# Kernel optimization log

Measured on AMD Instinct MI355X. Metric: run time of the kernel, lower is better.

Reference implementation:

```python
import jax, jax.numpy as jnp
import numpy as np

N_QUBITS = 12
RANK = 1024
K = 4            # outcomes per qubit
D = 2 ** N_QUBITS
N_IDX = 1_000_000


def setup_inputs() -> dict:
    key = jax.random.key(0)
    k1, k2, k3, k4 = jax.random.split(key, 4)
    params = jax.random.normal(k1, (2, D, RANK), dtype=jnp.float32)
    M_real = jax.random.normal(k2, (K, 2, 2), dtype=jnp.float32)
    M_imag = jax.random.normal(k3, (K, 2, 2), dtype=jnp.float32)
    P_idxs = jax.random.randint(k4, (N_IDX,), 0, K ** N_QUBITS, dtype=jnp.int64)
    return {"params": params, "M_real": M_real, "M_imag": M_imag, "P_idxs": P_idxs}


def _qmt(rho, M, n_qubits):
    """Born rule: P[s1..sN] = Tr[(M_{s1} x ... x M_{sN}) rho].
    Sequential per-qubit contraction; T has shape [K^n, 2^(N-n), 2^(N-n)]."""
    T = rho[None, :, :]  # axes: (done outcomes, row legs j, col legs i)
    for _ in range(n_qubits):
        k, r, c = T.shape[0], T.shape[1] // 2, T.shape[2] // 2
        Tt = T.reshape(k, 2, r, 2, c)  # (k, j_n, j_rest, i_n, i_rest)
        # Tr contribution: sum_{i,j} M[s,i,j] * rho[j,i]
        T = jnp.einsum('sij,kjait->ksat', M, Tt).reshape(k * M.shape[0], r, c)
    return T.reshape(-1)  # [K^N] complex


def reference(params, M_real, M_imag, P_idxs):
    # rho = U U^H / Tr(U U^H)
    U = jax.lax.complex(params[0], params[1])            # [D, RANK] complex64
    rho = U @ U.conj().T                                  # [D, D]
    rho = rho / jnp.trace(rho)
    M = jax.lax.complex(M_real, M_imag)                   # [K, 2, 2] complex64
    P_all = _qmt(rho, M, N_QUBITS).real                   # [K^N] float32
    return P_all[P_idxs]
```

## Files before the change

### kernel.cpp

```cpp
#include <hip/hip_runtime.h>

#define D 4096
#define RANK 1024
#define UELEMS 4194304ULL
#define NTOT 16777216ULL
#define QSCALE 16000.0f

typedef __attribute__((ext_vector_type(4))) int i32x4;

__device__ float g_inv_tr[1];
__device__ float g_scale[D];
__device__ float g_mdre[16];
__device__ float g_mdim[16];

static __device__ __forceinline__ void load_lds16(const void* g, void* l) {
    __builtin_amdgcn_global_load_lds(
        (const __attribute__((address_space(1))) unsigned int*)g,
        (__attribute__((address_space(3))) unsigned int*)l, 16, 0, 0);
}

#define MFMA_I8 __builtin_amdgcn_mfma_i32_16x16x64_i8

__global__ __launch_bounds__(256) void convert_w_i8(const float* __restrict__ P,
                                                    const float* __restrict__ Mre,
                                                    const float* __restrict__ Mim,
                                                    char* __restrict__ Wh,
                                                    char* __restrict__ Wl,
                                                    char* __restrict__ W2)
{
    if (blockIdx.x == 0 && threadIdx.x < 16) {
        const int s = threadIdx.x >> 2, i = (threadIdx.x >> 1) & 1, j = threadIdx.x & 1;
        g_mdre[threadIdx.x] =  Mre[s * 4 + j * 2 + i];
        g_mdim[threadIdx.x] = -Mim[s * 4 + j * 2 + i];
    }

    const int w = threadIdx.x >> 6, lane = threadIdx.x & 63;
    const int row = blockIdx.x * 4 + w;

    float ur[16], ui[16];
    const float* pr = P + (size_t)row * RANK + lane * 16;
    const float* pi = P + UELEMS + (size_t)row * RANK + lane * 16;
    #pragma unroll
    for (int q = 0; q < 4; ++q) {
        const float4 a = ((const float4*)pr)[q];
        const float4 b = ((const float4*)pi)[q];
        ur[q * 4 + 0] = a.x; ur[q * 4 + 1] = a.y; ur[q * 4 + 2] = a.z; ur[q * 4 + 3] = a.w;
        ui[q * 4 + 0] = b.x; ui[q * 4 + 1] = b.y; ui[q * 4 + 2] = b.z; ui[q * 4 + 3] = b.w;
    }
    float mx = 0.f;
    #pragma unroll
    for (int e = 0; e < 16; ++e)
        mx = fmaxf(mx, fmaxf(fabsf(ur[e]), fabsf(ui[e])));
    #pragma unroll
    for (int off = 1; off < 64; off <<= 1)
        mx = fmaxf(mx, __shfl_xor(mx, off));
    const float inv = mx > 0.f ? QSCALE / mx : 0.f;
    if (lane == 0) g_scale[row] = mx / QSCALE;

    int hr[16], lr[16], hi[16], li[16];
    #pragma unroll
    for (int e = 0; e < 16; ++e) {
        float q = ur[e] * inv;
        float hf = rintf(q * 0.0078125f);
        hr[e] = (int)hf; lr[e] = (int)rintf(q - 128.f * hf);
        q = ui[e] * inv;
        hf = rintf(q * 0.0078125f);
        hi[e] = (int)hf; li[e] = (int)rintf(q - 128.f * hf);
    }
    uint4 phr, plr, phi, pli;
    unsigned* dst[4] = {(unsigned*)&phr, (unsigned*)&plr, (unsigned*)&phi, (unsigned*)&pli};
    #pragma unroll
    for (int q = 0; q < 4; ++q) {
        unsigned a = 0, b = 0, c = 0, d = 0;
        #pragma unroll
        for (int k = 0; k < 4; ++k) {
            const int sh = k * 8;
            a |= (unsigned)(hr[q * 4 + k] & 255) << sh;
            b |= (unsigned)(lr[q * 4 + k] & 255) << sh;
            c |= (unsigned)(hi[q * 4 + k] & 255) << sh;
            d |= (unsigned)(li[q * 4 + k] & 255) << sh;
        }
        dst[0][q] = a; dst[1][q] = b; dst[2][q] = c; dst[3][q] = d;
    }
    const size_t b1 = (size_t)row * 2048 + lane * 16;
    *(uint4*)&Wh[b1] = phr;          *(uint4*)&Wl[b1] = plr;
    *(uint4*)&Wh[b1 + 1024] = phi;   *(uint4*)&Wl[b1 + 1024] = pli;

    const size_t b2 = ((size_t)lane * 4096 + row) * 16;
    *(uint4*)&W2[b2]                = phr;
    *(uint4*)&W2[b2 + 4194304]      = plr;
    *(uint4*)&W2[b2 + 8388608]      = phi;
    *(uint4*)&W2[b2 + 12582912]     = pli;
}

__global__ __launch_bounds__(256, 2) void gemm_rho_i8(const char* __restrict__ Wh,
                                                      const char* __restrict__ Wl,
                                                      const char* __restrict__ W2,
                                                      float2* __restrict__ rho)
{
    __shared__ __align__(16) char sA[2][4][64 * 64];

    const int g0 = blockIdx.x;
    const int g = (g0 & 7) * 260 + (g0 >> 3);

    int bi = (int)((sqrtf(8.f * (float)g + 1.f) - 1.f) * 0.5f);
    while (bi * (bi + 1) / 2 > g) --bi;
    while ((bi + 1) * (bi + 2) / 2 <= g) ++bi;
    const int bj = g - bi * (bi + 1) / 2;
    const int row0 = bi << 6, col0 = bj << 6;

    const int t = threadIdx.x;
    const int lane = t & 63, w = t >> 6;
    const int wr = w >> 1, wc = w & 1;

    const int ra = t >> 2;
    const int kca = (t & 3) ^ ((ra >> 1) & 3);
    const size_t aoff = (size_t)(row0 + ra) * 2048 + kca * 16;
    const int ldso = t * 16;

    const int m = lane & 15, gq = lane >> 4;
    const int fko = (gq ^ ((m >> 1) & 3)) * 16;

    const size_t bcol = ((size_t)gq * 4096 + col0 + wc * 32 + m) * 16;

    i32x4 rehh[2][2], remx[2][2], iphh[2][2], ipmx[2][2], iqhh[2][2], iqmx[2][2];
    #pragma unroll
    for (int i = 0; i < 2; ++i)
        #pragma unroll
        for (int j = 0; j < 2; ++j) {
            rehh[i][j] = (i32x4){0, 0, 0, 0}; remx[i][j] = (i32x4){0, 0, 0, 0};
            iphh[i][j] = (i32x4){0, 0, 0, 0}; ipmx[i][j] = (i32x4){0, 0, 0, 0};
            iqhh[i][j] = (i32x4){0, 0, 0, 0}; iqmx[i][j] = (i32x4){0, 0, 0, 0};
        }

    char* const sA0 = &sA[0][0][0];

#define STAGE_A(bn, kt)                                                       \
    {                                                                         \
        const size_t ko_ = (size_t)(kt) * 64;                                 \
        char* dA_ = sA0 + (bn) * 16384;                                       \
        load_lds16(Wh + aoff + ko_,        dA_ + ldso);                       \
        load_lds16(Wl + aoff + ko_,        dA_ + 4096  + ldso);               \
        load_lds16(Wh + aoff + ko_ + 1024, dA_ + 8192  + ldso);               \
        load_lds16(Wl + aoff + ko_ + 1024, dA_ + 12288 + ldso);               \
    }

    STAGE_A(0, 0)
    __syncthreads();

    #pragma unroll 2
    for (int kt = 0; kt < 16; ++kt) {
        const int cur = kt & 1;
        const char* sAc = sA0 + cur * 16384;

        i32x4 b1h[2], b1l[2], b2h[2], b2l[2];
        {
            const char* pB = W2 + bcol + (size_t)kt * 262144;
            #pragma unroll
            for (int j = 0; j < 2; ++j) {
                b1h[j] = *(const i32x4*)(pB + j * 256);
                b1l[j] = *(const i32x4*)(pB + 4194304  + j * 256);
                b2h[j] = *(const i32x4*)(pB + 8388608  + j * 256);
                b2l[j] = *(const i32x4*)(pB + 12582912 + j * 256);
            }
        }

        if (kt < 15) STAGE_A(cur ^ 1, kt + 1)

        i32x4 fa1h[2], fa1l[2], fa2h[2], fa2l[2];
        #pragma unroll
        for (int i = 0; i < 2; ++i) {
            const int off = (wr * 32 + i * 16 + m) * 64 + fko;
            fa1h[i] = *(const i32x4*)(sAc + off);
            fa1l[i] = *(const i32x4*)(sAc + 4096  + off);
            fa2h[i] = *(const i32x4*)(sAc + 8192  + off);
            fa2l[i] = *(const i32x4*)(sAc + 12288 + off);
        }

        __builtin_amdgcn_s_setprio(1);
        #pragma unroll
        for (int j = 0; j < 2; ++j)
            #pragma unroll
            for (int i = 0; i < 2; ++i) {
                i32x4 r;
                r = rehh[i][j];
                r = MFMA_I8(fa1h[i], b1h[j], r, 0, 0, 0);
                r = MFMA_I8(fa2h[i], b2h[j], r, 0, 0, 0);
                rehh[i][j] = r;
                r = remx[i][j];
                r = MFMA_I8(fa1h[i], b1l[j], r, 0, 0, 0);
                r = MFMA_I8(fa1l[i], b1h[j], r, 0, 0, 0);
                r = MFMA_I8(fa2h[i], b2l[j], r, 0, 0, 0);
                r = MFMA_I8(fa2l[i], b2h[j], r, 0, 0, 0);
                remx[i][j] = r;
                r = MFMA_I8(fa2h[i], b1h[j], iphh[i][j], 0, 0, 0);
                iphh[i][j] = r;
                r = ipmx[i][j];
                r = MFMA_I8(fa2h[i], b1l[j], r, 0, 0, 0);
                r = MFMA_I8(fa2l[i], b1h[j], r, 0, 0, 0);
                ipmx[i][j] = r;
                r = MFMA_I8(fa1h[i], b2h[j], iqhh[i][j], 0, 0, 0);
                iqhh[i][j] = r;
                r = iqmx[i][j];
                r = MFMA_I8(fa1h[i], b2l[j], r, 0, 0, 0);
                r = MFMA_I8(fa1l[i], b2h[j], r, 0, 0, 0);
                iqmx[i][j] = r;
            }
        __builtin_amdgcn_s_setprio(0);

        __syncthreads();
    }
#undef STAGE_A

    #pragma unroll
    for (int j = 0; j < 2; ++j) {
        const int col = col0 + wc * 32 + j * 16 + m;
        const float sc = g_scale[col];
        const int c64 = col >> 6;
        #pragma unroll
        for (int i = 0; i < 2; ++i) {
            #pragma unroll
            for (int r = 0; r < 4; ++r) {
                const int row = row0 + wr * 32 + i * 16 + gq * 4 + r;
                const float s2 = g_scale[row] * sc;
                const float re = s2 * (16384.f * (float)rehh[i][j][r] + 128.f * (float)remx[i][j][r]);
                const float im = s2 * (16384.f * (float)(iphh[i][j][r] - iqhh[i][j][r])
                                      + 128.f * (float)(ipmx[i][j][r] - iqmx[i][j][r]));
                const int r64 = row >> 6;
                if (r64 > c64 || row >= col) rho[(size_t)row * D + col] = make_float2(re, im);
                if (r64 == c64 && row > col) rho[(size_t)col * D + row] = make_float2(re, -im);
            }
        }
    }
}

__global__ void trace_inv(const float2* __restrict__ rho)
{
    __shared__ float red[256];
    float s = 0.f;
    for (int d = threadIdx.x; d < D; d += 256)
        s += rho[(size_t)d * (D + 1)].x;
    red[threadIdx.x] = s;
    __syncthreads();
    for (int off = 128; off > 0; off >>= 1) {
        if (threadIdx.x < off) red[threadIdx.x] += red[threadIdx.x + off];
        __syncthreads();
    }
    if (threadIdx.x == 0) g_inv_tr[0] = 1.0f / red[0];
}

static __device__ __forceinline__ void qmt2(float2* x,
                                            const float* __restrict__ Mre,
                                            const float* __restrict__ Mim)
{
    float2 y[16];
    #pragma unroll
    for (int sb = 0; sb < 4; ++sb)
        #pragma unroll
        for (int ja = 0; ja < 2; ++ja)
            #pragma unroll
            for (int ia = 0; ia < 2; ++ia) {
                float2 acc = make_float2(0.f, 0.f);
                #pragma unroll
                for (int ib = 0; ib < 2; ++ib)
                    #pragma unroll
                    for (int jb = 0; jb < 2; ++jb) {
                        const float mr = Mre[sb * 4 + ib * 2 + jb];
                        const float mi = Mim[sb * 4 + ib * 2 + jb];
                        const float2 v = x[(ja * 2 + jb) * 4 + ia * 2 + ib];
                        acc.x += mr * v.x - mi * v.y;
                        acc.y += mr * v.y + mi * v.x;
                    }
                y[sb * 4 + ja * 2 + ia] = acc;
            }
    #pragma unroll
    for (int sa = 0; sa < 4; ++sa)
        #pragma unroll
        for (int sb = 0; sb < 4; ++sb) {
            float2 acc = make_float2(0.f, 0.f);
            #pragma unroll
            for (int ia = 0; ia < 2; ++ia)
                #pragma unroll
                for (int ja = 0; ja < 2; ++ja) {
                    const float mr = Mre[sa * 4 + ia * 2 + ja];
                    const float mi = Mim[sa * 4 + ia * 2 + ja];
                    const float2 v = y[sb * 4 + ja * 2 + ia];
                    acc.x += mr * v.x - mi * v.y;
                    acc.y += mr * v.y + mi * v.x;
                }
            x[sa * 4 + sb] = acc;
        }
}

static __device__ __forceinline__ void pA_pipeline(float2* x, float2* X, const int t,
                                                   const float* __restrict__ mre,
                                                   const float* __restrict__ mim)
{
    qmt2(x, mre, mim);
    #pragma unroll
    for (int d = 0; d < 16; ++d) X[t * 17 + d] = x[d];
    __syncthreads();
    const int a2 = t >> 6, t2 = (t >> 4) & 3, d1 = t & 15;
    #pragma unroll
    for (int j2 = 0; j2 < 4; ++j2)
        #pragma unroll
        for (int i2 = 0; i2 < 4; ++i2)
            x[j2 * 4 + i2] = X[((a2 * 4 + j2) * 16 + t2 * 4 + i2) * 17 + d1];
    __syncthreads();
    qmt2(x, mre, mim);
    #pragma unroll
    for (int d = 0; d < 16; ++d) X[(a2 * 4 + t2) * 257 + d * 16 + d1] = x[d];
    __syncthreads();
    const int e2 = t >> 4, e1 = t & 15;
    #pragma unroll
    for (int j2 = 0; j2 < 4; ++j2)
        #pragma unroll
        for (int i2 = 0; i2 < 4; ++i2)
            x[j2 * 4 + i2] = X[(j2 * 4 + i2) * 257 + e2 * 16 + e1];
    qmt2(x, mre, mim);
}

__global__ __launch_bounds__(256) void qmt_pAh(const float2* __restrict__ in,
                                               float2* __restrict__ out,
                                               const float* __restrict__ Mre,
                                               const float* __restrict__ Mim)
{
    __shared__ __align__(16) float2 X[256 * 17];
    const int t = threadIdx.x;
    const int g = blockIdx.x;
    int rr = (int)((sqrtf(8.f * (float)g + 1.f) - 1.f) * 0.5f);
    while (rr * (rr + 1) / 2 > g) --rr;
    while ((rr + 1) * (rr + 2) / 2 <= g) ++rr;
    const int cc = g - rr * (rr + 1) / 2;

    const int a4 = t >> 4, t4 = t & 15;
    float2 x0[16], x[16];
    #pragma unroll
    for (int j2 = 0; j2 < 4; ++j2) {
        const float2* p = in + ((size_t)(rr * 64 + a4 * 4 + j2)) * 4096 + cc * 64 + t4 * 4;
        const float4 v0 = ((const float4*)p)[0];
        const float4 v1 = ((const float4*)p)[1];
        x0[j2 * 4 + 0] = make_float2(v0.x, v0.y);
        x0[j2 * 4 + 1] = make_float2(v0.z, v0.w);
        x0[j2 * 4 + 2] = make_float2(v1.x, v1.y);
        x0[j2 * 4 + 3] = make_float2(v1.z, v1.w);
    }

    #pragma unroll
    for (int q = 0; q < 16; ++q) x[q] = x0[q];
    pA_pipeline(x, X, t, Mre, Mim);
    const int e2 = t >> 4, e1 = t & 15;
    const size_t ob0 = (size_t)(rr * 64 + cc) * 4096 + e2 * 16 + e1;
    #pragma unroll
    for (int d = 0; d < 16; ++d) out[ob0 + (size_t)d * 256] = x[d];

    if (rr != cc) {
        __syncthreads();
        #pragma unroll
        for (int q = 0; q < 16; ++q) x[q] = x0[q];
        pA_pipeline(x, X, t, g_mdre, g_mdim);
        const size_t ob1 = (size_t)(cc * 64 + rr) * 4096 + e2 * 16 + e1;
        #pragma unroll
        for (int d = 0; d < 16; ++d)
            out[ob1 + (size_t)d * 256] = make_float2(x[d].x, -x[d].y);
    }
}

static __device__ __forceinline__ void qmt_stage_cb_half(float2* x,
                                                         const float* __restrict__ Mre,
                                                         const float* __restrict__ Mim)
{
    #pragma unroll
    for (int jb = 0; jb < 2; ++jb) {
        float2 y[16];
        #pragma unroll
        for (int sc = 0; sc < 4; ++sc)
            #pragma unroll
            for (int ii = 0; ii < 4; ++ii) {
                float2 acc = make_float2(0.f, 0.f);
                #pragma unroll
                for (int ic = 0; ic < 2; ++ic)
                    #pragma unroll
                    for (int jc = 0; jc < 2; ++jc) {
                        const float mr = Mre[sc * 4 + ic * 2 + jc];
                        const float mi = Mim[sc * 4 + ic * 2 + jc];
                        const float2 v = x[jb * 16 + jc * 8 + ii * 2 + ic];
                        acc.x += mr * v.x - mi * v.y;
                        acc.y += mr * v.y + mi * v.x;
                    }
                y[sc * 4 + ii] = acc;
            }
        #pragma unroll
        for (int q = 0; q < 16; ++q) x[jb * 16 + q] = y[q];
    }
    #pragma unroll
    for (int sc = 0; sc < 4; ++sc) {
        float2 z[8];
        #pragma unroll
        for (int sb = 0; sb < 4; ++sb)
            #pragma unroll
            for (int ia = 0; ia < 2; ++ia) {
                float2 acc = make_float2(0.f, 0.f);
                #pragma unroll
                for (int ib = 0; ib < 2; ++ib)
                    #pragma unroll
                    for (int jb = 0; jb < 2; ++jb) {
                        const float mr = Mre[sb * 4 + ib * 2 + jb];
                        const float mi = Mim[sb * 4 + ib * 2 + jb];
                        const float2 v = x[jb * 16 + sc * 4 + ia * 2 + ib];
                        acc.x += mr * v.x - mi * v.y;
                        acc.y += mr * v.y + mi * v.x;
                    }
                z[sb * 2 + ia] = acc;
            }
        #pragma unroll
        for (int sb = 0; sb < 4; ++sb)
            #pragma unroll
            for (int ia = 0; ia < 2; ++ia)
                x[(sb >> 1) * 16 + sc * 4 + ia * 2 + (sb & 1)] = z[sb * 2 + ia];
    }
}

#define STAGE_A_COEFFS                                                        \
    float Are[2][2], Aim[2][2], Bre[2][2], Bim[2][2];                         \
    _Pragma("unroll")                                                         \
    for (int sal = 0; sal < 2; ++sal)                                         \
        _Pragma("unroll")                                                     \
        for (int ia = 0; ia < 2; ++ia) {                                      \
            const int sa = 2 * h + sal;                                       \
            Are[sal][ia] = Mre[sa * 4 + ia * 2 + h];                          \
            Aim[sal][ia] = Mim[sa * 4 + ia * 2 + h];                          \
            Bre[sal][ia] = Mre[sa * 4 + ia * 2 + (1 - h)];                    \
            Bim[sal][ia] = Mim[sa * 4 + ia * 2 + (1 - h)];                    \
        }

__global__ __launch_bounds__(256) void qmt_p3(const float2* __restrict__ in,
                                              float2* __restrict__ out,
                                              const float* __restrict__ Mre,
                                              const float* __restrict__ Mim)
{
    const int t = threadIdx.x;
    const int h = (t >> 5) & 1;
    const int idx = blockIdx.x * 4 + (t >> 6);
    const int rc = idx >> 7;
    const int r3 = rc >> 3, c3 = rc & 7;
    const int s = (idx & 127) * 32 + (t & 31);

    float2 x[32];
    #pragma unroll
    for (int jb = 0; jb < 2; ++jb)
        #pragma unroll
        for (int jc = 0; jc < 2; ++jc) {
            const int j3 = 4 * h + 2 * jb + jc;
            #pragma unroll
            for (int i3 = 0; i3 < 8; ++i3)
                x[jb * 16 + jc * 8 + i3] =
                    in[(size_t)((r3 * 8 + j3) * 64 + c3 * 8 + i3) * 4096 + s];
        }

    qmt_stage_cb_half(x, Mre, Mim);

    STAGE_A_COEFFS
    const size_t ob = ((size_t)(r3 * 8 + c3) * 64) * 4096 + s;
    #pragma unroll
    for (int sbH = 0; sbH < 2; ++sbH)
        #pragma unroll
        for (int sc = 0; sc < 4; ++sc)
            #pragma unroll
            for (int sbL = 0; sbL < 2; ++sbL) {
                const int q = sbH * 16 + sc * 4 + sbL;
                const float2 o0 = x[q], o1 = x[q + 2];
                float2 r0, r1;
                r0.x = __shfl_xor(o0.x, 32); r0.y = __shfl_xor(o0.y, 32);
                r1.x = __shfl_xor(o1.x, 32); r1.y = __shfl_xor(o1.y, 32);
                const int sb = sbH * 2 + sbL;
                #pragma unroll
                for (int sal = 0; sal < 2; ++sal) {
                    const float re = Are[sal][0] * o0.x - Aim[sal][0] * o0.y
                                   + Are[sal][1] * o1.x - Aim[sal][1] * o1.y
                                   + Bre[sal][0] * r0.x - Bim[sal][0] * r0.y
                                   + Bre[sal][1] * r1.x - Bim[sal][1] * r1.y;
                    const float im = Are[sal][0] * o0.y + Aim[sal][0] * o0.x
                                   + Are[sal][1] * o1.y + Aim[sal][1] * o1.x
                                   + Bre[sal][0] * r0.y + Bim[sal][0] * r0.x
                                   + Bre[sal][1] * r1.y + Bim[sal][1] * r1.x;
                    const int s3 = (2 * h + sal) * 16 + sb * 4 + sc;
                    out[ob + (size_t)s3 * 4096] = make_float2(re, im);
                }
            }
}

__global__ __launch_bounds__(256) void qmt_p4(const float2* __restrict__ in,
                                              float* __restrict__ out,
                                              const float* __restrict__ Mre,
                                              const float* __restrict__ Mim)
{
    const int t = threadIdx.x;
    const int h = (t >> 5) & 1;
    const int s = (blockIdx.x * 4 + (t >> 6)) * 32 + (t & 31);

    float2 x[32];
    #pragma unroll
    for (int jb = 0; jb < 2; ++jb)
        #pragma unroll
        for (int jc = 0; jc < 2; ++jc) {
            const int j3 = 4 * h + 2 * jb + jc;
            #pragma unroll
            for (int i3 = 0; i3 < 8; ++i3)
                x[jb * 16 + jc * 8 + i3] = in[(size_t)(j3 * 8 + i3) * 262144 + s];
        }

    qmt_stage_cb_half(x, Mre, Mim);

    STAGE_A_COEFFS
    const size_t ob = (size_t)(s >> 5) * 2048 + (s & 31);
    #pragma unroll
    for (int sbH = 0; sbH < 2; ++sbH)
        #pragma unroll
        for (int sc = 0; sc < 4; ++sc)
            #pragma unroll
            for (int sbL = 0; sbL < 2; ++sbL) {
                const int q = sbH * 16 + sc * 4 + sbL;
                const float2 o0 = x[q], o1 = x[q + 2];
                float2 r0, r1;
                r0.x = __shfl_xor(o0.x, 32); r0.y = __shfl_xor(o0.y, 32);
                r1.x = __shfl_xor(o1.x, 32); r1.y = __shfl_xor(o1.y, 32);
                const int sb = sbH * 2 + sbL;
                #pragma unroll
                for (int sal = 0; sal < 2; ++sal) {
                    const float re = Are[sal][0] * o0.x - Aim[sal][0] * o0.y
                                   + Are[sal][1] * o1.x - Aim[sal][1] * o1.y
                                   + Bre[sal][0] * r0.x - Bim[sal][0] * r0.y
                                   + Bre[sal][1] * r1.x - Bim[sal][1] * r1.y;
                    const int s3 = (2 * h + sal) * 16 + sb * 4 + sc;
                    out[ob + (size_t)s3 * 32] = re;
                }
            }
}

__global__ void gather_idx(const float* __restrict__ P, const int* __restrict__ idxs,
                           float* __restrict__ out, const int n)
{
    const int i = blockIdx.x * 256 + threadIdx.x;
    if (i < n) {
        const int idx = idxs[i];
        const int s = idx & 262143;
        const size_t pos = (size_t)(s >> 5) * 2048 + (size_t)(idx >> 18) * 32 + (s & 31);
        out[i] = P[pos] * g_inv_tr[0];
    }
}

extern "C" void kernel_launch(void* const* d_in, const int* in_sizes, int n_in,
                              void* d_out, int out_size, void* d_ws, size_t ws_size,
                              hipStream_t stream)
{
    const float* params = (const float*)d_in[0];
    const float* Mre    = (const float*)d_in[1];
    const float* Mim    = (const float*)d_in[2];
    const int*   idxs   = (const int*)d_in[3];
    float*       out    = (float*)d_out;

    float* ws = (float*)d_ws;
    float2* A  = (float2*)ws;
    float2* Bp = (float2*)(ws + 2 * NTOT);
    char* Wh = (char*)Bp;
    char* Wl = Wh + (size_t)D * 2048;
    char* W2 = Wl + (size_t)D * 2048;

    convert_w_i8<<<1024, 256, 0, stream>>>(params, Mre, Mim, Wh, Wl, W2);
    gemm_rho_i8<<<2080, 256, 0, stream>>>(Wh, Wl, W2, A);
    trace_inv<<<1, 256, 0, stream>>>(A);

    qmt_pAh<<<2080, 256, 0, stream>>>(A, Bp, Mre, Mim);
    qmt_p3<<<2048, 256, 0, stream>>>(Bp, A, Mre, Mim);
    qmt_p4<<<2048, 256, 0, stream>>>(A, (float*)Bp, Mre, Mim);

    gather_idx<<<(out_size + 255) / 256, 256, 0, stream>>>((float*)Bp, idxs, out, out_size);
}
```

Measured before the change: 412.4 us.

## Load GEMM A fragments directly from global W2 layout, drop LDS staging

The rho GEMM no longer stages the A operand through double-buffered LDS with global_load_lds. Both A and B fragments are now read directly from the transposed W2 layout in global memory, so the row-major Wh/Wl copies and their writes in the convert kernel are removed. This cuts the conversion kernel's write traffic and removes the per-iteration barriers and LDS traffic. In exchange, A loads now go to global/L2 per wave with no explicit prefetch overlap, which may expose memory latency in the MFMA loop.

```diff
diff --git a/kernel.cpp b/kernel.cpp
--- a/kernel.cpp
+++ b/kernel.cpp
@@ -13,19 +13,11 @@
 __device__ float g_mdre[16];
 __device__ float g_mdim[16];
 
-static __device__ __forceinline__ void load_lds16(const void* g, void* l) {
-    __builtin_amdgcn_global_load_lds(
-        (const __attribute__((address_space(1))) unsigned int*)g,
-        (__attribute__((address_space(3))) unsigned int*)l, 16, 0, 0);
-}
-
 #define MFMA_I8 __builtin_amdgcn_mfma_i32_16x16x64_i8
 
 __global__ __launch_bounds__(256) void convert_w_i8(const float* __restrict__ P,
                                                     const float* __restrict__ Mre,
                                                     const float* __restrict__ Mim,
-                                                    char* __restrict__ Wh,
-                                                    char* __restrict__ Wl,
                                                     char* __restrict__ W2)
 {
     if (blockIdx.x == 0 && threadIdx.x < 16) {
@@ -82,24 +74,17 @@
         }
         dst[0][q] = a; dst[1][q] = b; dst[2][q] = c; dst[3][q] = d;
     }
-    const size_t b1 = (size_t)row * 2048 + lane * 16;
-    *(uint4*)&Wh[b1] = phr;          *(uint4*)&Wl[b1] = plr;
-    *(uint4*)&Wh[b1 + 1024] = phi;   *(uint4*)&Wl[b1 + 1024] = pli;
 
     const size_t b2 = ((size_t)lane * 4096 + row) * 16;
-    *(uint4*)&W2[b2]                = phr;
-    *(uint4*)&W2[b2 + 4194304]      = plr;
-    *(uint4*)&W2[b2 + 8388608]      = phi;
-    *(uint4*)&W2[b2 + 12582912]     = pli;
-}
-
-__global__ __launch_bounds__(256, 2) void gemm_rho_i8(const char* __restrict__ Wh,
-                                                      const char* __restrict__ Wl,
-                                                      const char* __restrict__ W2,
+    *(uint4*)&W2[b2]            = phr;
+    *(uint4*)&W2[b2 + 4194304]  = plr;
+    *(uint4*)&W2[b2 + 8388608]  = phi;
+    *(uint4*)&W2[b2 + 12582912] = pli;
+}
+
+__global__ __launch_bounds__(256, 2) void gemm_rho_i8(const char* __restrict__ W2,
                                                       float2* __restrict__ rho)
 {
-    __shared__ __align__(16) char sA[2][4][64 * 64];
-
     const int g0 = blockIdx.x;
     const int g = (g0 & 7) * 260 + (g0 >> 3);
 
@@ -113,15 +98,10 @@
     const int lane = t & 63, w = t >> 6;
     const int wr = w >> 1, wc = w & 1;
 
-    const int ra = t >> 2;
-    const int kca = (t & 3) ^ ((ra >> 1) & 3);
-    const size_t aoff = (size_t)(row0 + ra) * 2048 + kca * 16;
-    const int ldso = t * 16;
-
     const int m = lane & 15, gq = lane >> 4;
-    const int fko = (gq ^ ((m >> 1) & 3)) * 16;
-
-    const size_t bcol = ((size_t)gq * 4096 + col0 + wc * 32 + m) * 16;
+
+    const char* pa = W2 + ((size_t)gq * 4096 + row0 + wr * 32 + m) * 16;
+    const char* pb = W2 + ((size_t)gq * 4096 + col0 + wc * 32 + m) * 16;
 
     i32x4 rehh[2][2], remx[2][2], iphh[2][2], ipmx[2][2], iqhh[2][2], iqmx[2][2];
     #pragma unroll
@@ -133,84 +113,57 @@
             iqhh[i][j] = (i32x4){0, 0, 0, 0}; iqmx[i][j] = (i32x4){0, 0, 0, 0};
         }
 
-    char* const sA0 = &sA[0][0][0];
-
-#define STAGE_A(bn, kt)                                                       \
-    {                                                                         \
-        const size_t ko_ = (size_t)(kt) * 64;                                 \
-        char* dA_ = sA0 + (bn) * 16384;                                       \
-        load_lds16(Wh + aoff + ko_,        dA_ + ldso);                       \
-        load_lds16(Wl + aoff + ko_,        dA_ + 4096  + ldso);               \
-        load_lds16(Wh + aoff + ko_ + 1024, dA_ + 8192  + ldso);               \
-        load_lds16(Wl + aoff + ko_ + 1024, dA_ + 12288 + ldso);               \
-    }
-
-    STAGE_A(0, 0)
-    __syncthreads();
-
-    #pragma unroll 2
+    #pragma unroll 4
     for (int kt = 0; kt < 16; ++kt) {
-        const int cur = kt & 1;
-        const char* sAc = sA0 + cur * 16384;
-
+        const char* pA = pa + (size_t)kt * 262144;
+        const char* pB = pb + (size_t)kt * 262144;
+
+        i32x4 a1h[2], a1l[2], a2h[2], a2l[2];
         i32x4 b1h[2], b1l[2], b2h[2], b2l[2];
-        {
-            const char* pB = W2 + bcol + (size_t)kt * 262144;
-            #pragma unroll
-            for (int j = 0; j < 2; ++j) {
-                b1h[j] = *(const i32x4*)(pB + j * 256);
-                b1l[j] = *(const i32x4*)(pB + 4194304  + j * 256);
-                b2h[j] = *(const i32x4*)(pB + 8388608  + j * 256);
-                b2l[j] = *(const i32x4*)(pB + 12582912 + j * 256);
-            }
-        }
-
-        if (kt < 15) STAGE_A(cur ^ 1, kt + 1)
-
-        i32x4 fa1h[2], fa1l[2], fa2h[2], fa2l[2];
         #pragma unroll
         for (int i = 0; i < 2; ++i) {
-            const int off = (wr * 32 + i * 16 + m) * 64 + fko;
-            fa1h[i] = *(const i32x4*)(sAc + off);
-            fa1l[i] = *(const i32x4*)(sAc + 4096  + off);
-            fa2h[i] = *(const i32x4*)(sAc + 8192  + off);
-            fa2l[i] = *(const i32x4*)(sAc + 12288 + off);
-        }
-
-        __builtin_amdgcn_s_setprio(1);
+            a1h[i] = *(const i32x4*)(pA + i * 256);
+            a1l[i] = *(const i32x4*)(pA + 4194304  + i * 256);
+            a2h[i] = *(const i32x4*)(pA + 8388608  + i * 256);
+            a2l[i] = *(const i32x4*)(pA + 12582912 + i * 256);
+        }
+        #pragma unroll
+        for (int j = 0; j < 2; ++j) {
+            b1h[j] = *(const i32x4*)(pB + j * 256);
+            b1l[j] = *(const i32x4*)(pB + 4194304  + j * 256);
+            b2h[j] = *(const i32x4*)(pB + 8388608  + j * 256);
+            b2l[j] = *(const i32x4*)(pB + 12582912 + j * 256);
+        }
+
         #pragma unroll
         for (int j = 0; j < 2; ++j)
             #pragma unroll
             for (int i = 0; i < 2; ++i) {
                 i32x4 r;
                 r = rehh[i][j];
-                r = MFMA_I8(fa1h[i], b1h[j], r, 0, 0, 0);
-                r = MFMA_I8(fa2h[i], b2h[j], r, 0, 0, 0);
+                r = MFMA_I8(a1h[i], b1h[j], r, 0, 0, 0);
+                r = MFMA_I8(a2h[i], b2h[j], r, 0, 0, 0);
                 rehh[i][j] = r;
                 r = remx[i][j];
-                r = MFMA_I8(fa1h[i], b1l[j], r, 0, 0, 0);
-                r = MFMA_I8(fa1l[i], b1h[j], r, 0, 0, 0);
-                r = MFMA_I8(fa2h[i], b2l[j], r, 0, 0, 0);
-                r = MFMA_I8(fa2l[i], b2h[j], r, 0, 0, 0);
+                r = MFMA_I8(a1h[i], b1l[j], r, 0, 0, 0);
+                r = MFMA_I8(a1l[i], b1h[j], r, 0, 0, 0);
+                r = MFMA_I8(a2h[i], b2l[j], r, 0, 0, 0);
+                r = MFMA_I8(a2l[i], b2h[j], r, 0, 0, 0);
                 remx[i][j] = r;
-                r = MFMA_I8(fa2h[i], b1h[j], iphh[i][j], 0, 0, 0);
+                r = MFMA_I8(a2h[i], b1h[j], iphh[i][j], 0, 0, 0);
                 iphh[i][j] = r;
                 r = ipmx[i][j];
-                r = MFMA_I8(fa2h[i], b1l[j], r, 0, 0, 0);
-                r = MFMA_I8(fa2l[i], b1h[j], r, 0, 0, 0);
+                r = MFMA_I8(a2h[i], b1l[j], r, 0, 0, 0);
+                r = MFMA_I8(a2l[i], b1h[j], r, 0, 0, 0);
                 ipmx[i][j] = r;
-                r = MFMA_I8(fa1h[i], b2h[j], iqhh[i][j], 0, 0, 0);
+                r = MFMA_I8(a1h[i], b2h[j], iqhh[i][j], 0, 0, 0);
                 iqhh[i][j] = r;
                 r = iqmx[i][j];
-                r = MFMA_I8(fa1h[i], b2l[j], r, 0, 0, 0);
-                r = MFMA_I8(fa1l[i], b2h[j], r, 0, 0, 0);
+                r = MFMA_I8(a1h[i], b2l[j], r, 0, 0, 0);
+                r = MFMA_I8(a1l[i], b2h[j], r, 0, 0, 0);
                 iqmx[i][j] = r;
             }
-        __builtin_amdgcn_s_setprio(0);
-
-        __syncthreads();
-    }
-#undef STAGE_A
+    }
 
     #pragma unroll
     for (int j = 0; j < 2; ++j) {
@@ -563,12 +516,10 @@
     float* ws = (float*)d_ws;
     float2* A  = (float2*)ws;
     float2* Bp = (float2*)(ws + 2 * NTOT);
-    char* Wh = (char*)Bp;
-    char* Wl = Wh + (size_t)D * 2048;
-    char* W2 = Wl + (size_t)D * 2048;
-
-    convert_w_i8<<<1024, 256, 0, stream>>>(params, Mre, Mim, Wh, Wl, W2);
-    gemm_rho_i8<<<2080, 256, 0, stream>>>(Wh, Wl, W2, A);
+    char* W2 = (char*)Bp;
+
+    convert_w_i8<<<1024, 256, 0, stream>>>(params, Mre, Mim, W2);
+    gemm_rho_i8<<<2080, 256, 0, stream>>>(W2, A);
     trace_inv<<<1, 256, 0, stream>>>(A);
 
     qmt_pAh<<<2080, 256, 0, stream>>>(A, Bp, Mre, Mim);
```

Result: slower. 427.5 us (+3.7%).
